# Optimization experiments

Measured on AMD Instinct MI355X. Metric: run time of the kernel, lower is better.

## Reference

```python
import jax, jax.numpy as jnp
import numpy as np

K = 32
D = 256


def setup_inputs() -> dict:
    key = jax.random.key(0)
    k1, k2, kW, kV, kb = jax.random.split(key, 5)
    B, L1, L2 = 16, 256, 256
    x1 = jax.random.normal(k1, (B, L1, D), dtype=jnp.float32)
    x2 = jax.random.normal(k2, (B, L2, D), dtype=jnp.float32)
    # kaiming_uniform-style init bounds
    bound_W = np.sqrt(6.0 / ((1 + 5) * D))  # fan_in = d, a=sqrt(5)
    W = jax.random.uniform(kW, (K, D, D), minval=-bound_W, maxval=bound_W, dtype=jnp.float32)
    bound_V = np.sqrt(6.0 / ((1 + 5) * 2 * D))
    V = jax.random.uniform(kV, (K, 2 * D), minval=-bound_V, maxval=bound_V, dtype=jnp.float32)
    bound_b = 1.0 / np.sqrt(2 * D)
    b = jax.random.uniform(kb, (K,), minval=-bound_b, maxval=bound_b, dtype=jnp.float32)
    return {"x1": x1, "x2": x2, "W": W, "V": V, "b": b}


def reference(x1, x2, W, V, b):
    # x1: [B,L1,d], x2: [B,L2,d], W: [k,d,d], V: [k,2d], b: [k]
    d = x1.shape[-1]
    # bilinear term: (x1 W) x2^T per output channel k -> [B,k,L1,L2]
    temp = jnp.einsum('bld,kde->bkle', x1, W)            # [B,k,L1,d]
    bilinear_out = jnp.einsum('bkle,bme->bklm', temp, x2)  # [B,k,L1,L2]
    # linear term: V @ concat(x1,x2) = V1 x1 + V2 x2, broadcast-summed
    V1, V2 = V[:, :d], V[:, d:]
    lin1 = jnp.einsum('bld,kd->bkl', x1, V1)             # [B,k,L1]
    lin2 = jnp.einsum('bmd,kd->bkm', x2, V2)             # [B,k,L2]
    linear_out = lin1[:, :, :, None] + lin2[:, :, None, :] + b[None, :, None, None]
    return jax.nn.relu(bilinear_out + linear_out)
```

## Files before the change

kernel.cpp:

```cpp
#include <hip/hip_runtime.h>
#include <hip/hip_bf16.h>

typedef unsigned short u16;
typedef unsigned short ushort8v __attribute__((ext_vector_type(8)));
typedef __bf16 bf16x8 __attribute__((ext_vector_type(8)));
typedef float f32x4 __attribute__((ext_vector_type(4)));

#define NB 16
#define NK 32
#define ND 256
#define NL 256

__device__ __forceinline__ u16 f2bf(float f) {
    __hip_bfloat16 h = __float2bfloat16(f);
    return __builtin_bit_cast(u16, h);
}

__device__ __forceinline__ void gload_lds16(const void* g, void* l) {
    __builtin_amdgcn_global_load_lds(
        (const __attribute__((address_space(1))) unsigned int*)g,
        (__attribute__((address_space(3))) unsigned int*)l, 16, 0, 0);
}


__global__ void prep_kernel(const float* __restrict__ x1, const float* __restrict__ x2,
                            const float* __restrict__ W,
                            u16* __restrict__ x1f, u16* __restrict__ x2f, u16* __restrict__ Wtf) {
    __shared__ float xs[32 * 260];
    int bid = blockIdx.x;
    int tid = threadIdx.x;
    if (bid < 2048) {
        const float* src; u16* dst; long f4;
        if (bid < 1024) { src = x1; dst = x1f; f4 = (long)bid * 256 + tid; }
        else            { src = x2; dst = x2f; f4 = (long)(bid - 1024) * 256 + tid; }
        long idx = f4 << 2;
        int mat = (int)(idx >> 16);
        int r = (int)((idx >> 8) & 255);
        int c = (int)(idx & 255);
        float4 v = ((const float4*)src)[f4];
        ushort4 o;
        o.x = f2bf(v.x); o.y = f2bf(v.y); o.z = f2bf(v.z); o.w = f2bf(v.w);
        int rt = r >> 4, ct = c >> 5;
        int lane = (r & 15) | (((c >> 3) & 3) << 4);
        long off = ((long)mat << 16) + (((rt << 3) + ct) << 9) + (lane << 3) + (c & 7);
        *(ushort4*)(dst + off) = o;
        return;
    }
    int wb = bid - 2048;
    int k  = wb >> 3;
    int dg = wb & 7;
    const float* wsrc = W + ((long)k << 16) + ((long)dg << 13);
#pragma unroll
    for (int it = 0; it < 8; ++it) {
        int ch = (it << 8) + tid;
        int row = ch >> 6;
        int col4 = ch & 63;
        float4 v = *(const float4*)(wsrc + (row << 8) + (col4 << 2));
        *(float4*)(xs + row * 260 + (col4 << 2)) = v;
    }
    __syncthreads();
    int e = tid;
    int rt = e >> 4;
    u16* wdst = Wtf + ((long)k << 16) + ((long)((rt << 3) + dg) << 9);
#pragma unroll
    for (int g = 0; g < 4; ++g) {
        ushort8v pk;
#pragma unroll
        for (int q = 0; q < 8; ++q)
            pk[q] = f2bf(xs[((g << 3) + q) * 260 + e]);
        *(ushort8v*)(wdst + (((e & 15) | (g << 4)) << 3)) = pk;
    }
}

__launch_bounds__(512, 4)
__global__ void ntn_main(const u16* __restrict__ x1f, const u16* __restrict__ x2f,
                         const u16* __restrict__ Wtf,
                         const float* __restrict__ V, const float* __restrict__ bb,
                         float* __restrict__ out) {
    __shared__ __align__(16) char ldsA[32768];
    __shared__ __align__(16) char ldsT[32768];
    __shared__ float r1[64];

    int bid = blockIdx.x;
    int xcd   = bid & 7;
    int j     = bid >> 3;
    int slot  = j >> 7;
    int inner = j & 127;
    int st    = (slot << 3) | xcd;
    int kg = st >> 2, bg = st & 3;
    int k  = (kg << 3) | (inner >> 4);
    int b  = (bg << 2) | ((inner >> 2) & 3);
    int lq = inner & 3;

    int tid  = threadIdx.x;
    int lane = tid & 63;
    int wid  = tid >> 6;
    int wm = wid >> 1;
    int wl = wid & 1;
    int lrow = lane & 15;
    int j4   = (lane >> 4) << 2;
    int lk8  = (lane >> 4) << 3;

    const u16* wtp = Wtf + ((long)k << 16);
    const u16* x2p = x2f + ((long)b << 16);

    {
        const char* src = (const char*)(x1f + ((long)b << 16) + ((long)lq << 14));
#pragma unroll
        for (int it = 0; it < 4; ++it) {
            int chunk = (it << 3) + wid;
            gload_lds16(src + (chunk << 10) + (lane << 4), ldsA + (chunk << 10));
        }
    }
    bf16x8 afC[4], afN[4];
#pragma unroll
    for (int q = 0; q < 4; ++q)
        afC[q] = *(const bf16x8*)(wtp + ((((wm << 2) + q) << 3) << 9) + (lane << 3));
    float bk = bb[k];
    __syncthreads();

    {
        int ll = tid >> 3;
        int et8 = tid & 7;
        const float* v1p = V + ((long)k << 9) + (et8 << 5);
        float s = 0.f;
#pragma unroll
        for (int eg = 0; eg < 4; ++eg) {
            int lp = (ll & 15) | (eg << 4);
            bf16x8 xv = *(const bf16x8*)(ldsA + ((((ll >> 4) << 3) + et8) << 10) + (lp << 4));
            float4 va = *(const float4*)(v1p + (eg << 3));
            float4 vb = *(const float4*)(v1p + (eg << 3) + 4);
            s += (float)xv[0] * va.x + (float)xv[1] * va.y + (float)xv[2] * va.z + (float)xv[3] * va.w
               + (float)xv[4] * vb.x + (float)xv[5] * vb.y + (float)xv[6] * vb.z + (float)xv[7] * vb.w;
        }
        s += __shfl_xor(s, 1);
        s += __shfl_xor(s, 2);
        s += __shfl_xor(s, 4);
        if ((tid & 7) == 0) r1[ll] = s + bk;
    }

    const f32x4 fz = {0.f, 0.f, 0.f, 0.f};
    f32x4 acc[4][2];
#pragma unroll
    for (int q = 0; q < 4; ++q) { acc[q][0] = fz; acc[q][1] = fz; }

    {
        bf16x8 bflC[2], bflN[2];
#pragma unroll
        for (int p = 0; p < 2; ++p)
            bflC[p] = *(const bf16x8*)(ldsA + (((((wl << 1) + p) << 3) << 10) + (lane << 4)));
#pragma unroll
        for (int dt = 0; dt < 8; ++dt) {
            if (dt < 7) {
#pragma unroll
                for (int q = 0; q < 4; ++q)
                    afN[q] = *(const bf16x8*)(wtp + (((((wm << 2) + q) << 3) + dt + 1) << 9) + (lane << 3));
#pragma unroll
                for (int p = 0; p < 2; ++p)
                    bflN[p] = *(const bf16x8*)(ldsA + ((((((wl << 1) + p) << 3) + dt + 1) << 10) + (lane << 4)));
            }
#pragma unroll
            for (int p = 0; p < 2; ++p)
#pragma unroll
                for (int q = 0; q < 4; ++q)
                    acc[q][p] = __builtin_amdgcn_mfma_f32_16x16x32_bf16(afC[q], bflC[p], acc[q][p], 0, 0, 0);
#pragma unroll
            for (int q = 0; q < 4; ++q) afC[q] = afN[q];
#pragma unroll
            for (int p = 0; p < 2; ++p) bflC[p] = bflN[p];
        }
    }
    __syncthreads();

    {
        const float* v2base = V + ((long)k << 9) + 256;
#pragma unroll
        for (int q = 0; q < 4; ++q) {
            int e0 = (wm << 6) + (q << 4) + j4;
            float4 v2q = *(const float4*)(v2base + e0);
#pragma unroll
            for (int p = 0; p < 2; ++p) {
                int l = (wl << 5) + (p << 4) + lrow;
                ushort4 pk;
                pk.x = f2bf(acc[q][p][0] + v2q.x);
                pk.y = f2bf(acc[q][p][1] + v2q.y);
                pk.z = f2bf(acc[q][p][2] + v2q.z);
                pk.w = f2bf(acc[q][p][3] + v2q.w);
                *(ushort4*)(ldsT + (l << 9) + ((e0 << 1) ^ ((l & 7) << 4))) = pk;
            }
        }
    }
    bf16x8 amC[4], amN[4];
#pragma unroll
    for (int q = 0; q < 4; ++q)
        amC[q] = *(const bf16x8*)(x2p + ((((wm << 2) + q) << 3) << 9) + (lane << 3));
    __syncthreads();

#pragma unroll
    for (int q = 0; q < 4; ++q) { acc[q][0] = fz; acc[q][1] = fz; }

    {
        bf16x8 tfC[2], tfN[2];
#pragma unroll
        for (int p = 0; p < 2; ++p) {
            int l = (wl << 5) + (p << 4) + lrow;
            tfC[p] = *(const bf16x8*)(ldsT + (l << 9) + ((lk8 << 1) ^ ((l & 7) << 4)));
        }
#pragma unroll
        for (int et = 0; et < 8; ++et) {
            if (et < 7) {
                int e = ((et + 1) << 5) + lk8;
#pragma unroll
                for (int q = 0; q < 4; ++q)
                    amN[q] = *(const bf16x8*)(x2p + (((((wm << 2) + q) << 3) + et + 1) << 9) + (lane << 3));
#pragma unroll
                for (int p = 0; p < 2; ++p) {
                    int l = (wl << 5) + (p << 4) + lrow;
                    tfN[p] = *(const bf16x8*)(ldsT + (l << 9) + ((e << 1) ^ ((l & 7) << 4)));
                }
            }
#pragma unroll
            for (int p = 0; p < 2; ++p)
#pragma unroll
                for (int q = 0; q < 4; ++q)
                    acc[q][p] = __builtin_amdgcn_mfma_f32_16x16x32_bf16(amC[q], tfC[p], acc[q][p], 0, 0, 0);
#pragma unroll
            for (int q = 0; q < 4; ++q) amC[q] = amN[q];
#pragma unroll
            for (int p = 0; p < 2; ++p) tfC[p] = tfN[p];
        }
    }

    {
        float* outp = out + (((long)(b * NK + k)) << 16) + ((long)(lq << 6) << 8);
#pragma unroll
        for (int c = 0; c < 2; ++c) {
            if (wl == c) {
#pragma unroll
                for (int q = 0; q < 4; ++q) {
                    int m0 = (wm << 6) + (q << 4) + j4;
#pragma unroll
                    for (int p = 0; p < 2; ++p) {
                        int row = (p << 4) + lrow;
                        float rb = r1[(c << 5) + row];
                        f32x4 v;
                        v[0] = acc[q][p][0] + rb;
                        v[1] = acc[q][p][1] + rb;
                        v[2] = acc[q][p][2] + rb;
                        v[3] = acc[q][p][3] + rb;
                        v[0] = v[0] > 0.f ? v[0] : 0.f;
                        v[1] = v[1] > 0.f ? v[1] : 0.f;
                        v[2] = v[2] > 0.f ? v[2] : 0.f;
                        v[3] = v[3] > 0.f ? v[3] : 0.f;
                        *(f32x4*)(ldsA + (row << 10) + ((m0 << 2) ^ ((row & 7) << 4))) = v;
                    }
                }
            }
            __syncthreads();
#pragma unroll
            for (int it = 0; it < 4; ++it) {
                int g = (it << 9) + tid;
                int row = g >> 6;
                int c4  = g & 63;
                f32x4 v = *(const f32x4*)(ldsA + (row << 10) + ((c4 << 4) ^ ((row & 7) << 4)));
                *(f32x4*)(outp + ((long)((c << 5) + row) << 8) + (c4 << 2)) = v;
            }
            if (c == 0) __syncthreads();
        }
    }
}

extern "C" void kernel_launch(void* const* d_in, const int* in_sizes, int n_in,
                              void* d_out, int out_size, void* d_ws, size_t ws_size,
                              hipStream_t stream) {
    const float* x1 = (const float*)d_in[0];
    const float* x2 = (const float*)d_in[1];
    const float* W  = (const float*)d_in[2];
    const float* V  = (const float*)d_in[3];
    const float* bb = (const float*)d_in[4];
    float* out = (float*)d_out;

    char* ws = (char*)d_ws;
    u16*   x1f  = (u16*)(ws);
    u16*   x2f  = (u16*)(ws + (2l << 20));
    u16*   Wtf  = (u16*)(ws + (4l << 20));

    hipLaunchKernelGGL(prep_kernel, dim3(2304), dim3(256), 0, stream,
                       x1, x2, W, x1f, x2f, Wtf);
    hipLaunchKernelGGL(ntn_main, dim3(2048), dim3(512), 0, stream,
                       x1f, x2f, Wtf, V, bb, out);
}
```

Measured before the change: 73.57 us.

## Process four output channels per block, reusing x1 tile, with LDS-only barriers

Each block now loops over four k channels instead of one. The x1 tile is loaded into LDS once and reused by all four channels, and the grid shrinks from 2048 to 512 blocks with a new block-to-(k,b,lq) mapping. The linear x1·V1 terms for all four channels are computed up front into a per-channel shared array. The output staging moves from ldsA to ldsT so the x1 tile stays resident. Block barriers now wait only on LDS counters, so outstanding global stores can overlap with later compute. The cost is fewer blocks in flight, which means less parallel slack and latency hiding, and a longer serial body per block.

```diff
diff --git a/kernel.cpp b/kernel.cpp
--- a/kernel.cpp
+++ b/kernel.cpp
@@ -20,6 +20,12 @@
     __builtin_amdgcn_global_load_lds(
         (const __attribute__((address_space(1))) unsigned int*)g,
         (__attribute__((address_space(3))) unsigned int*)l, 16, 0, 0);
+}
+
+__device__ __forceinline__ void barrier_lgkm() {
+    asm volatile("s_waitcnt lgkmcnt(0)" ::: "memory");
+    __builtin_amdgcn_s_barrier();
+    asm volatile("" ::: "memory");
 }
 
 
@@ -79,18 +85,14 @@
                          float* __restrict__ out) {
     __shared__ __align__(16) char ldsA[32768];
     __shared__ __align__(16) char ldsT[32768];
-    __shared__ float r1[64];
+    __shared__ float r1s[4][64];
 
     int bid = blockIdx.x;
-    int xcd   = bid & 7;
-    int j     = bid >> 3;
-    int slot  = j >> 7;
-    int inner = j & 127;
-    int st    = (slot << 3) | xcd;
-    int kg = st >> 2, bg = st & 3;
-    int k  = (kg << 3) | (inner >> 4);
-    int b  = (bg << 2) | ((inner >> 2) & 3);
-    int lq = inner & 3;
+    int xcd = bid & 7;
+    int i   = bid >> 3;
+    int kg  = ((xcd >> 1) << 1) | (i >> 5);
+    int b   = ((xcd & 1) << 3) | ((i >> 2) & 7);
+    int lq  = i & 3;
 
     int tid  = threadIdx.x;
     int lane = tid & 63;
@@ -101,7 +103,6 @@
     int j4   = (lane >> 4) << 2;
     int lk8  = (lane >> 4) << 3;
 
-    const u16* wtp = Wtf + ((long)k << 16);
     const u16* x2p = x2f + ((long)b << 16);
 
     {
@@ -112,160 +113,166 @@
             gload_lds16(src + (chunk << 10) + (lane << 4), ldsA + (chunk << 10));
         }
     }
-    bf16x8 afC[4], afN[4];
-#pragma unroll
-    for (int q = 0; q < 4; ++q)
-        afC[q] = *(const bf16x8*)(wtp + ((((wm << 2) + q) << 3) << 9) + (lane << 3));
-    float bk = bb[k];
     __syncthreads();
 
     {
         int ll = tid >> 3;
         int et8 = tid & 7;
-        const float* v1p = V + ((long)k << 9) + (et8 << 5);
-        float s = 0.f;
-#pragma unroll
-        for (int eg = 0; eg < 4; ++eg) {
-            int lp = (ll & 15) | (eg << 4);
-            bf16x8 xv = *(const bf16x8*)(ldsA + ((((ll >> 4) << 3) + et8) << 10) + (lp << 4));
-            float4 va = *(const float4*)(v1p + (eg << 3));
-            float4 vb = *(const float4*)(v1p + (eg << 3) + 4);
-            s += (float)xv[0] * va.x + (float)xv[1] * va.y + (float)xv[2] * va.z + (float)xv[3] * va.w
-               + (float)xv[4] * vb.x + (float)xv[5] * vb.y + (float)xv[6] * vb.z + (float)xv[7] * vb.w;
-        }
-        s += __shfl_xor(s, 1);
-        s += __shfl_xor(s, 2);
-        s += __shfl_xor(s, 4);
-        if ((tid & 7) == 0) r1[ll] = s + bk;
+#pragma unroll
+        for (int ki = 0; ki < 4; ++ki) {
+            int kk = (kg << 2) + ki;
+            const float* v1p = V + ((long)kk << 9) + (et8 << 5);
+            float s = 0.f;
+#pragma unroll
+            for (int eg = 0; eg < 4; ++eg) {
+                int lp = (ll & 15) | (eg << 4);
+                bf16x8 xv = *(const bf16x8*)(ldsA + ((((ll >> 4) << 3) + et8) << 10) + (lp << 4));
+                float4 va = *(const float4*)(v1p + (eg << 3));
+                float4 vb = *(const float4*)(v1p + (eg << 3) + 4);
+                s += (float)xv[0] * va.x + (float)xv[1] * va.y + (float)xv[2] * va.z + (float)xv[3] * va.w
+                   + (float)xv[4] * vb.x + (float)xv[5] * vb.y + (float)xv[6] * vb.z + (float)xv[7] * vb.w;
+            }
+            s += __shfl_xor(s, 1);
+            s += __shfl_xor(s, 2);
+            s += __shfl_xor(s, 4);
+            if ((tid & 7) == 0) r1s[ki][ll] = s + bb[kk];
+        }
     }
 
     const f32x4 fz = {0.f, 0.f, 0.f, 0.f};
-    f32x4 acc[4][2];
-#pragma unroll
-    for (int q = 0; q < 4; ++q) { acc[q][0] = fz; acc[q][1] = fz; }
-
-    {
-        bf16x8 bflC[2], bflN[2];
-#pragma unroll
-        for (int p = 0; p < 2; ++p)
-            bflC[p] = *(const bf16x8*)(ldsA + (((((wl << 1) + p) << 3) << 10) + (lane << 4)));
-#pragma unroll
-        for (int dt = 0; dt < 8; ++dt) {
-            if (dt < 7) {
-#pragma unroll
-                for (int q = 0; q < 4; ++q)
-                    afN[q] = *(const bf16x8*)(wtp + (((((wm << 2) + q) << 3) + dt + 1) << 9) + (lane << 3));
+
+    for (int ki = 0; ki < 4; ++ki) {
+        int k = (kg << 2) + ki;
+        const u16* wtp = Wtf + ((long)k << 16);
+
+        f32x4 acc[4][2];
+#pragma unroll
+        for (int q = 0; q < 4; ++q) { acc[q][0] = fz; acc[q][1] = fz; }
+        {
+            bf16x8 afC[4], afN[4], bflC[2], bflN[2];
+#pragma unroll
+            for (int q = 0; q < 4; ++q)
+                afC[q] = *(const bf16x8*)(wtp + ((((wm << 2) + q) << 3) << 9) + (lane << 3));
+#pragma unroll
+            for (int p = 0; p < 2; ++p)
+                bflC[p] = *(const bf16x8*)(ldsA + (((((wl << 1) + p) << 3) << 10) + (lane << 4)));
+#pragma unroll
+            for (int dt = 0; dt < 8; ++dt) {
+                if (dt < 7) {
+#pragma unroll
+                    for (int q = 0; q < 4; ++q)
+                        afN[q] = *(const bf16x8*)(wtp + (((((wm << 2) + q) << 3) + dt + 1) << 9) + (lane << 3));
+#pragma unroll
+                    for (int p = 0; p < 2; ++p)
+                        bflN[p] = *(const bf16x8*)(ldsA + ((((((wl << 1) + p) << 3) + dt + 1) << 10) + (lane << 4)));
+                }
 #pragma unroll
                 for (int p = 0; p < 2; ++p)
-                    bflN[p] = *(const bf16x8*)(ldsA + ((((((wl << 1) + p) << 3) + dt + 1) << 10) + (lane << 4)));
-            }
-#pragma unroll
-            for (int p = 0; p < 2; ++p)
-#pragma unroll
-                for (int q = 0; q < 4; ++q)
-                    acc[q][p] = __builtin_amdgcn_mfma_f32_16x16x32_bf16(afC[q], bflC[p], acc[q][p], 0, 0, 0);
-#pragma unroll
-            for (int q = 0; q < 4; ++q) afC[q] = afN[q];
-#pragma unroll
-            for (int p = 0; p < 2; ++p) bflC[p] = bflN[p];
-        }
-    }
-    __syncthreads();
-
-    {
-        const float* v2base = V + ((long)k << 9) + 256;
-#pragma unroll
-        for (int q = 0; q < 4; ++q) {
-            int e0 = (wm << 6) + (q << 4) + j4;
-            float4 v2q = *(const float4*)(v2base + e0);
+#pragma unroll
+                    for (int q = 0; q < 4; ++q)
+                        acc[q][p] = __builtin_amdgcn_mfma_f32_16x16x32_bf16(afC[q], bflC[p], acc[q][p], 0, 0, 0);
+#pragma unroll
+                for (int q = 0; q < 4; ++q) afC[q] = afN[q];
+#pragma unroll
+                for (int p = 0; p < 2; ++p) bflC[p] = bflN[p];
+            }
+        }
+        barrier_lgkm();
+
+        {
+            const float* v2base = V + ((long)k << 9) + 256;
+#pragma unroll
+            for (int q = 0; q < 4; ++q) {
+                int e0 = (wm << 6) + (q << 4) + j4;
+                float4 v2q = *(const float4*)(v2base + e0);
+#pragma unroll
+                for (int p = 0; p < 2; ++p) {
+                    int l = (wl << 5) + (p << 4) + lrow;
+                    ushort4 pk;
+                    pk.x = f2bf(acc[q][p][0] + v2q.x);
+                    pk.y = f2bf(acc[q][p][1] + v2q.y);
+                    pk.z = f2bf(acc[q][p][2] + v2q.z);
+                    pk.w = f2bf(acc[q][p][3] + v2q.w);
+                    *(ushort4*)(ldsT + (l << 9) + ((e0 << 1) ^ ((l & 7) << 4))) = pk;
+                }
+            }
+        }
+        barrier_lgkm();
+
+#pragma unroll
+        for (int q = 0; q < 4; ++q) { acc[q][0] = fz; acc[q][1] = fz; }
+        {
+            bf16x8 amC[4], amN[4], tfC[2], tfN[2];
+#pragma unroll
+            for (int q = 0; q < 4; ++q)
+                amC[q] = *(const bf16x8*)(x2p + ((((wm << 2) + q) << 3) << 9) + (lane << 3));
 #pragma unroll
             for (int p = 0; p < 2; ++p) {
                 int l = (wl << 5) + (p << 4) + lrow;
-                ushort4 pk;
-                pk.x = f2bf(acc[q][p][0] + v2q.x);
-                pk.y = f2bf(acc[q][p][1] + v2q.y);
-                pk.z = f2bf(acc[q][p][2] + v2q.z);
-                pk.w = f2bf(acc[q][p][3] + v2q.w);
-                *(ushort4*)(ldsT + (l << 9) + ((e0 << 1) ^ ((l & 7) << 4))) = pk;
-            }
-        }
-    }
-    bf16x8 amC[4], amN[4];
-#pragma unroll
-    for (int q = 0; q < 4; ++q)
-        amC[q] = *(const bf16x8*)(x2p + ((((wm << 2) + q) << 3) << 9) + (lane << 3));
-    __syncthreads();
-
-#pragma unroll
-    for (int q = 0; q < 4; ++q) { acc[q][0] = fz; acc[q][1] = fz; }
-
-    {
-        bf16x8 tfC[2], tfN[2];
-#pragma unroll
-        for (int p = 0; p < 2; ++p) {
-            int l = (wl << 5) + (p << 4) + lrow;
-            tfC[p] = *(const bf16x8*)(ldsT + (l << 9) + ((lk8 << 1) ^ ((l & 7) << 4)));
-        }
-#pragma unroll
-        for (int et = 0; et < 8; ++et) {
-            if (et < 7) {
-                int e = ((et + 1) << 5) + lk8;
-#pragma unroll
-                for (int q = 0; q < 4; ++q)
-                    amN[q] = *(const bf16x8*)(x2p + (((((wm << 2) + q) << 3) + et + 1) << 9) + (lane << 3));
-#pragma unroll
-                for (int p = 0; p < 2; ++p) {
-                    int l = (wl << 5) + (p << 4) + lrow;
-                    tfN[p] = *(const bf16x8*)(ldsT + (l << 9) + ((e << 1) ^ ((l & 7) << 4)));
-                }
-            }
-#pragma unroll
-            for (int p = 0; p < 2; ++p)
-#pragma unroll
-                for (int q = 0; q < 4; ++q)
-                    acc[q][p] = __builtin_amdgcn_mfma_f32_16x16x32_bf16(amC[q], tfC[p], acc[q][p], 0, 0, 0);
-#pragma unroll
-            for (int q = 0; q < 4; ++q) amC[q] = amN[q];
-#pragma unroll
-            for (int p = 0; p < 2; ++p) tfC[p] = tfN[p];
-        }
-    }
-
-    {
-        float* outp = out + (((long)(b * NK + k)) << 16) + ((long)(lq << 6) << 8);
-#pragma unroll
-        for (int c = 0; c < 2; ++c) {
-            if (wl == c) {
-#pragma unroll
-                for (int q = 0; q < 4; ++q) {
-                    int m0 = (wm << 6) + (q << 4) + j4;
+                tfC[p] = *(const bf16x8*)(ldsT + (l << 9) + ((lk8 << 1) ^ ((l & 7) << 4)));
+            }
+#pragma unroll
+            for (int et = 0; et < 8; ++et) {
+                if (et < 7) {
+                    int e = ((et + 1) << 5) + lk8;
+#pragma unroll
+                    for (int q = 0; q < 4; ++q)
+                        amN[q] = *(const bf16x8*)(x2p + (((((wm << 2) + q) << 3) + et + 1) << 9) + (lane << 3));
 #pragma unroll
                     for (int p = 0; p < 2; ++p) {
-                        int row = (p << 4) + lrow;
-                        float rb = r1[(c << 5) + row];
-                        f32x4 v;
-                        v[0] = acc[q][p][0] + rb;
-                        v[1] = acc[q][p][1] + rb;
-                        v[2] = acc[q][p][2] + rb;
-                        v[3] = acc[q][p][3] + rb;
-                        v[0] = v[0] > 0.f ? v[0] : 0.f;
-                        v[1] = v[1] > 0.f ? v[1] : 0.f;
-                        v[2] = v[2] > 0.f ? v[2] : 0.f;
-                        v[3] = v[3] > 0.f ? v[3] : 0.f;
-                        *(f32x4*)(ldsA + (row << 10) + ((m0 << 2) ^ ((row & 7) << 4))) = v;
+                        int l = (wl << 5) + (p << 4) + lrow;
+                        tfN[p] = *(const bf16x8*)(ldsT + (l << 9) + ((e << 1) ^ ((l & 7) << 4)));
                     }
                 }
-            }
-            __syncthreads();
-#pragma unroll
-            for (int it = 0; it < 4; ++it) {
-                int g = (it << 9) + tid;
-                int row = g >> 6;
-                int c4  = g & 63;
-                f32x4 v = *(const f32x4*)(ldsA + (row << 10) + ((c4 << 4) ^ ((row & 7) << 4)));
-                *(f32x4*)(outp + ((long)((c << 5) + row) << 8) + (c4 << 2)) = v;
-            }
-            if (c == 0) __syncthreads();
+#pragma unroll
+                for (int p = 0; p < 2; ++p)
+#pragma unroll
+                    for (int q = 0; q < 4; ++q)
+                        acc[q][p] = __builtin_amdgcn_mfma_f32_16x16x32_bf16(amC[q], tfC[p], acc[q][p], 0, 0, 0);
+#pragma unroll
+                for (int q = 0; q < 4; ++q) amC[q] = amN[q];
+#pragma unroll
+                for (int p = 0; p < 2; ++p) tfC[p] = tfN[p];
+            }
+        }
+        barrier_lgkm();
+
+        {
+            float* outp = out + (((long)(b * NK + k)) << 16) + ((long)(lq << 6) << 8);
+#pragma unroll
+            for (int c = 0; c < 2; ++c) {
+                if (wl == c) {
+#pragma unroll
+                    for (int q = 0; q < 4; ++q) {
+                        int m0 = (wm << 6) + (q << 4) + j4;
+#pragma unroll
+                        for (int p = 0; p < 2; ++p) {
+                            int row = (p << 4) + lrow;
+                            float rb = r1s[ki][(c << 5) + row];
+                            f32x4 v;
+                            v[0] = acc[q][p][0] + rb;
+                            v[1] = acc[q][p][1] + rb;
+                            v[2] = acc[q][p][2] + rb;
+                            v[3] = acc[q][p][3] + rb;
+                            v[0] = v[0] > 0.f ? v[0] : 0.f;
+                            v[1] = v[1] > 0.f ? v[1] : 0.f;
+                            v[2] = v[2] > 0.f ? v[2] : 0.f;
+                            v[3] = v[3] > 0.f ? v[3] : 0.f;
+                            *(f32x4*)(ldsT + (row << 10) + ((m0 << 2) ^ ((row & 7) << 4))) = v;
+                        }
+                    }
+                }
+                barrier_lgkm();
+#pragma unroll
+                for (int it = 0; it < 4; ++it) {
+                    int g = (it << 9) + tid;
+                    int row = g >> 6;
+                    int c4  = g & 63;
+                    f32x4 v = *(const f32x4*)(ldsT + (row << 10) + ((c4 << 4) ^ ((row & 7) << 4)));
+                    *(f32x4*)(outp + ((long)((c << 5) + row) << 8) + (c4 << 2)) = v;
+                }
+                if (c == 0) barrier_lgkm();
+            }
         }
     }
 }
@@ -287,6 +294,6 @@
 
     hipLaunchKernelGGL(prep_kernel, dim3(2304), dim3(256), 0, stream,
                        x1, x2, W, x1f, x2f, Wtf);
-    hipLaunchKernelGGL(ntn_main, dim3(2048), dim3(512), 0, stream,
+    hipLaunchKernelGGL(ntn_main, dim3(512), dim3(512), 0, stream,
                        x1f, x2f, Wtf, V, bb, out);
 }
```

Result: slower. 105.3 us (+43.1%).
